# Optimization experiments

Measured on AMD Instinct MI355X. Metric: run time of the kernel, lower is better.

Reference implementation:

```python
import jax, jax.numpy as jnp
import numpy as np
from jax import lax

CUT = 20            # voxel grid per side, hard-coded in the torch module
N, P, OP = 32, 8192, 2048


def _w(key, shape, fan_in):
    return jax.random.normal(key, shape, dtype=jnp.float32) * np.float32(1.0 / np.sqrt(fan_in))


def setup_inputs() -> dict:
    key = jax.random.key(0)
    ks = jax.random.split(key, 20)
    inp = {}
    inp["sc"] = jax.random.uniform(ks[0], (N, P, 2), dtype=jnp.float32, minval=-0.5, maxval=0.5)
    inp["oc"] = jax.random.uniform(ks[1], (N, OP, 2), dtype=jnp.float32, minval=-0.5, maxval=0.5)
    inp["pos"] = jax.random.uniform(ks[2], (N, 2), dtype=jnp.float32, minval=-0.5, maxval=0.5)
    # voxel PointNet MLP (1x1 Conv1d == per-point linear)
    inp["mlp_w1"] = _w(ks[3], (128, 2), 2);        inp["mlp_b1"] = jnp.zeros((128,), jnp.float32)
    inp["mlp_w2"] = _w(ks[4], (256, 128), 128);    inp["mlp_b2"] = jnp.zeros((256,), jnp.float32)
    # dense conv pyramid
    inp["conv1_w"] = _w(ks[5], (512, 256, 3, 3), 256 * 9);   inp["conv1_b"] = jnp.zeros((512,), jnp.float32)
    inp["conv2_w"] = _w(ks[6], (1024, 512, 3, 3), 512 * 9);  inp["conv2_b"] = jnp.zeros((1024,), jnp.float32)
    inp["convt_w"] = _w(ks[7], (512, 1024, 2, 2), 1024 * 4); inp["convt_b"] = jnp.zeros((512,), jnp.float32)
    # object set-abstraction (stack of 1x1 Conv1d)
    inp["sa_w1"] = _w(ks[8], (64, 2), 2);          inp["sa_b1"] = jnp.zeros((64,), jnp.float32)
    inp["sa_w2"] = _w(ks[9], (128, 64), 64);       inp["sa_b2"] = jnp.zeros((128,), jnp.float32)
    inp["sa_w3"] = _w(ks[10], (256, 128), 128);    inp["sa_b3"] = jnp.zeros((256,), jnp.float32)
    inp["sa_w4"] = _w(ks[11], (512, 256), 256);    inp["sa_b4"] = jnp.zeros((512,), jnp.float32)
    # per-cell classifier
    inp["cls_w1"] = _w(ks[12], (1024, 1538), 1538); inp["cls_b1"] = jnp.zeros((1024,), jnp.float32)
    inp["cls_w2"] = _w(ks[13], (256, 1024), 1024);  inp["cls_b2"] = jnp.zeros((256,), jnp.float32)
    inp["cls_w3"] = _w(ks[14], (1, 256), 256);      inp["cls_b3"] = jnp.zeros((1,), jnp.float32)
    return inp


def _conv2d(x, w, b):
    y = lax.conv_general_dilated(x, w, (1, 1), ((1, 1), (1, 1)),
                                 dimension_numbers=("NCHW", "OIHW", "NCHW"))
    return y + b[None, :, None, None]


def _maxpool2(x):
    return lax.reduce_window(x, -jnp.inf, lax.max, (1, 1, 2, 2), (1, 1, 2, 2), "VALID")


def reference(sc, oc, pos,
              mlp_w1, mlp_b1, mlp_w2, mlp_b2,
              conv1_w, conv1_b, conv2_w, conv2_b, convt_w, convt_b,
              sa_w1, sa_b1, sa_w2, sa_b2, sa_w3, sa_b3, sa_w4, sa_b4,
              cls_w1, cls_b1, cls_w2, cls_b2, cls_w3, cls_b3):
    n = sc.shape[0]
    # ---- fused voxelization + PointNet + scatter-max (replaces triple loop) ----
    x, y = sc[..., 0], sc[..., 1]
    # torch condition: cut[i] < x <= cut[i+1] on linspace(-0.5, 0.5, 21)
    bi = jnp.clip(jnp.ceil((x + 0.5) * CUT) - 1, 0, CUT - 1).astype(jnp.int32)
    bj = jnp.clip(jnp.ceil((y + 0.5) * CUT) - 1, 0, CUT - 1).astype(jnp.int32)
    valid = (x > -0.5) & (x <= 0.5) & (y > -0.5) & (y <= 0.5)
    ci = -0.5 + (bi.astype(sc.dtype) + 0.5) / CUT   # voxel center x
    cj = -0.5 + (bj.astype(sc.dtype) + 0.5) / CUT   # voxel center y
    pc = jnp.stack([x - ci, y - cj], axis=-1).reshape(-1, 2)        # [n*P, 2]
    h = jax.nn.relu(pc @ mlp_w1.T + mlp_b1)
    feat = jax.nn.relu(h @ mlp_w2.T + mlp_b2)                       # [n*P, 256]
    seg = jnp.where(valid,
                    jnp.arange(n, dtype=jnp.int32)[:, None] * (CUT * CUT) + bi * CUT + bj,
                    n * CUT * CUT).reshape(-1)                      # invalid -> dummy bin
    nseg = n * CUT * CUT + 1
    mx = jax.ops.segment_max(feat, seg, num_segments=nseg)
    cnt = jax.ops.segment_sum(jnp.ones((n * P,), jnp.float32), seg, num_segments=nseg)
    vox = jnp.where(cnt[:, None] > 0, mx, 0.0)[: n * CUT * CUT]     # empty voxels stay 0
    vox = vox.reshape(n, CUT, CUT, 256).transpose(0, 3, 1, 2)       # [n,256,20,20]
    # ---- dense conv pyramid ----
    f1 = _maxpool2(jax.nn.relu(_conv2d(vox, conv1_w, conv1_b)))     # [n,512,10,10]
    f2 = _maxpool2(jax.nn.relu(_conv2d(f1, conv2_w, conv2_b)))      # [n,1024,5,5]
    f3 = lax.conv_transpose(f2, convt_w, (2, 2), "VALID",
                            dimension_numbers=("NCHW", "OIHW", "NCHW"))
    f3 = f3 + convt_b[None, :, None, None]                          # [n,512,10,10]
    scene = jnp.concatenate([f1, f3], axis=1)                       # [n,1024,10,10]
    S = scene.shape[2]
    scene_flat = scene.reshape(n, 1024, S * S)
    # ---- object PointNet (1x1 convs == per-point linears) + global max ----
    obj_c = oc - jnp.mean(oc, axis=1, keepdims=True)                # [n,OP,2]
    g = jax.nn.relu(obj_c @ sa_w1.T + sa_b1)
    g = jax.nn.relu(g @ sa_w2.T + sa_b2)
    g = jax.nn.relu(g @ sa_w3.T + sa_b3)
    g = jax.nn.relu(g @ sa_w4.T + sa_b4)                            # [n,OP,512]
    obj = jnp.max(g, axis=1)                                        # [n,512]
    obj_tiled = jnp.broadcast_to(obj[:, :, None], (n, 512, S * S))
    # ---- relative position grid ----
    c = -0.5 + (jnp.arange(S, dtype=sc.dtype) + 0.5) / S
    rel_x = jnp.broadcast_to(pos[:, 0][:, None, None] - c[None, :, None], (n, S, S))
    rel_y = jnp.broadcast_to(pos[:, 1][:, None, None] - c[None, None, :], (n, S, S))
    rel = jnp.stack([rel_x, rel_y], axis=1).reshape(n, 2, S * S)
    # ---- per-cell classifier ----
    cin = jnp.concatenate([scene_flat, obj_tiled, rel], axis=1).transpose(0, 2, 1)  # [n,100,1538]
    h = jax.nn.relu(cin @ cls_w1.T + cls_b1)
    h = jax.nn.relu(h @ cls_w2.T + cls_b2)
    return h @ cls_w3.T + cls_b3                                    # [n,100,1]
```

## Files before the change

### kernel.cpp

```cpp
#include <hip/hip_runtime.h>

#define NB 32
#define PP 8192
#define OPP 2048

typedef _Float16 f16;
typedef f16 half8 __attribute__((ext_vector_type(8)));
typedef f16 half4 __attribute__((ext_vector_type(4)));
typedef f16 half2v __attribute__((ext_vector_type(2)));
typedef float f32x4 __attribute__((ext_vector_type(4)));

#define MFMA16(a, b, c) __builtin_amdgcn_mfma_f32_16x16x32_f16(a, b, c, 0, 0, 0)

template <int CO, int CI>
__global__ __launch_bounds__(256) void wfragprep_k(const float* __restrict__ wsrc,
                                                   f16* __restrict__ wf) {
  __shared__ float tile[CI * 9];
  int co = blockIdx.x, t = threadIdx.x;
  const float* src = wsrc + (size_t)co * CI * 9;
  for (int i = t; i < CI * 9; i += 256) tile[i] = src[i];
  __syncthreads();
  constexpr int NBB = CO / 16;
  int nb = co >> 4, l16 = co & 15;
  for (int e = t; e < (CI / 32) * 9 * 4; e += 256) {
    int quad = e & 3;
    int kk = (e >> 2) % 9;
    int cic = e / 36;
    half8 v;
#pragma unroll
    for (int j = 0; j < 8; ++j) {
      int ci = cic * 32 + quad * 8 + j;
      v[j] = (f16)tile[ci * 9 + kk];
    }
    *(half8*)(wf + ((((size_t)cic * 9 + kk) * NBB + nb) * 64 + quad * 16 + l16) * 8) = v;
  }
}

__global__ void cvt16_k(const float* __restrict__ in, f16* __restrict__ out, int n4) {
  int idx = blockIdx.x * 256 + threadIdx.x;
  if (idx >= n4) return;
  float4 v = ((const float4*)in)[idx];
  half4 h; h.x = (f16)v.x; h.y = (f16)v.y; h.z = (f16)v.z; h.w = (f16)v.w;
  ((half4*)out)[idx] = h;
}

__global__ void cw1prep_k(const float* __restrict__ w, f16* __restrict__ out) {
  int idx = blockIdx.x * 256 + threadIdx.x;
  if (idx >= 1024 * 1024) return;
  int co = idx >> 10, k = idx & 1023;
  out[idx] = (f16)w[(size_t)co * 1538 + k];
}

__global__ void ctprep_k(const float* __restrict__ w, f16* __restrict__ out) {
  int idx = blockIdx.x * 256 + threadIdx.x;
  if (idx >= 2048 * 1024) return;
  int j = idx & 7, l = (idx >> 3) & 63, kb = (idx >> 9) & 31, nb = idx >> 14;
  int n16 = l & 15, quad = l >> 4;
  int np = nb * 16 + n16;
  int k = kb * 32 + quad * 8 + j;
  int p = np >> 9, o = np & 511;
  out[idx] = (f16)w[((size_t)o * 1024 + k) * 4 + (3 - p)];
}

__global__ void ocmean_k(const float* __restrict__ oc, float* __restrict__ ocm) {
  int n = blockIdx.x, t = threadIdx.x;
  __shared__ float sx[256], sy[256];
  float ax = 0.f, ay = 0.f;
  for (int p = t; p < OPP; p += 256) {
    ax += oc[((size_t)n * OPP + p) * 2 + 0];
    ay += oc[((size_t)n * OPP + p) * 2 + 1];
  }
  sx[t] = ax; sy[t] = ay;
  __syncthreads();
  for (int s = 128; s > 0; s >>= 1) {
    if (t < s) { sx[t] += sx[t + s]; sy[t] += sy[t + s]; }
    __syncthreads();
  }
  if (t == 0) {
    ocm[n * 2 + 0] = sx[0] / (float)OPP;
    ocm[n * 2 + 1] = sy[0] / (float)OPP;
  }
}

__global__ __launch_bounds__(256) void pointnet_lds_k(
    const float* __restrict__ sc, const float* __restrict__ w1, const float* __restrict__ b1,
    const f16* __restrict__ w2h, const float* __restrict__ b2, float* __restrict__ voxg) {
  __shared__ float voxl[400 * 33];
  int t = threadIdx.x, lane = t & 63, w = t >> 6;
  int quad = lane >> 4, l16 = lane & 15;
  int b = blockIdx.x;
  int ps = b & 3, cg = (b >> 2) & 7, n = b >> 5;
  half2v w1x2[16], w1y2[16], b12[16];
#pragma unroll
  for (int i = 0; i < 16; ++i) {
    int k0 = (i >> 2) * 32 + quad * 8 + (i & 3) * 2;
    w1x2[i] = (half2v){(f16)w1[k0 * 2], (f16)w1[(k0 + 1) * 2]};
    w1y2[i] = (half2v){(f16)w1[k0 * 2 + 1], (f16)w1[(k0 + 1) * 2 + 1]};
    b12[i]  = (half2v){(f16)b1[k0], (f16)b1[k0 + 1]};
  }
  half8 bf[2][4];
  float bias[2];
#pragma unroll
  for (int nt = 0; nt < 2; ++nt) {
    int ch = cg * 32 + nt * 16 + l16;
    bias[nt] = b2[ch];
#pragma unroll
    for (int ks = 0; ks < 4; ++ks)
      bf[nt][ks] = *(const half8*)(w2h + (size_t)ch * 128 + ks * 32 + quad * 8);
  }
  for (int i = t; i < 400 * 33; i += 256) voxl[i] = 0.0f;
  __syncthreads();
  const half2v z2 = {};
  const float* scp = sc + ((size_t)n * PP + (size_t)ps * 2048) * 2;
  int p0 = w * 16 + l16;
  float2 xy = *(const float2*)(scp + p0 * 2);
  for (int it = 0; it < 32; ++it) {
    float x = xy.x, y = xy.y;
    if (it < 31) xy = *(const float2*)(scp + ((it + 1) * 64 + p0) * 2);
    float bif = fminf(fmaxf(ceilf((x + 0.5f) * 20.0f) - 1.0f, 0.0f), 19.0f);
    float bjf = fminf(fmaxf(ceilf((y + 0.5f) * 20.0f) - 1.0f, 0.0f), 19.0f);
    bool valid = (x > -0.5f) && (x <= 0.5f) && (y > -0.5f) && (y <= 0.5f);
    float px = x - (-0.5f + (bif + 0.5f) * 0.05f);
    float py = y - (-0.5f + (bjf + 0.5f) * 0.05f);
    int bn = valid ? ((int)bif * 20 + (int)bjf) : -1;
    f16 pxh = (f16)px, pyh = (f16)py;
    half2v px2 = (half2v){pxh, pxh}, py2 = (half2v){pyh, pyh};
    f32x4 acc0 = {}, acc1 = {};
#pragma unroll
    for (int ks = 0; ks < 4; ++ks) {
      half8 af;
#pragma unroll
      for (int j2 = 0; j2 < 4; ++j2) {
        half2v tmp = w1x2[ks * 4 + j2] * px2 + (w1y2[ks * 4 + j2] * py2 + b12[ks * 4 + j2]);
        tmp = __builtin_elementwise_max(tmp, z2);
        reinterpret_cast<half2v*>(&af)[j2] = tmp;
      }
      acc0 = MFMA16(af, bf[0][ks], acc0);
      acc1 = MFMA16(af, bf[1][ks], acc1);
    }
#pragma unroll
    for (int r = 0; r < 4; ++r) {
      int bn2 = __shfl(bn, quad * 4 + r);
      if (bn2 >= 0) {
        float v0 = fmaxf(acc0[r] + bias[0], 0.0f);
        float v1 = fmaxf(acc1[r] + bias[1], 0.0f);
        atomicMax((int*)voxl + bn2 * 33 + l16, __float_as_int(v0));
        atomicMax((int*)voxl + bn2 * 33 + 16 + l16, __float_as_int(v1));
      }
    }
  }
  __syncthreads();
  float* vg = voxg + ((size_t)n * 400) * 256 + cg * 32;
  for (int i = t; i < 400 * 32; i += 256) {
    int bin = i >> 5, c = i & 31;
    float v = voxl[bin * 33 + c];
    if (v > 0.0f)
      atomicMax((int*)(vg + (size_t)bin * 256) + c, __float_as_int(v));
  }
}

template <int H, int W, int CI, int CO, int MSPLIT>
__global__ __launch_bounds__(256, 2) void convmfma_k(
    const f16* __restrict__ inh, const f16* __restrict__ wf,
    const float* __restrict__ bias, f16* __restrict__ outh) {
  constexpr int HS = H / MSPLIT;
  constexpr int Mpix = HS * W;
  constexpr int MT = (Mpix + 15) / 16;
  constexpr int PR = HS + 2, PC = W + 2;
  constexpr int NCIC = CI / 32;
  constexpr int COG = CO / 128;
  constexpr int NBB = CO / 16;
  extern __shared__ char smem[];
  f16* Ap = (f16*)smem;
  int b = blockIdx.x;
  int cog = b % COG;
  int ms = (b / COG) % MSPLIT;
  int n = b / (COG * MSPLIT);
  int co0 = cog * 128;
  int r0 = ms * HS;
  int t = threadIdx.x, lane = t & 63, w = t >> 6;
  int quad = lane >> 4, l16 = lane & 15;
  int nb0 = cog * 8 + w * 2;

  int abase[MT];
#pragma unroll
  for (int mi = 0; mi < MT; ++mi) {
    int pl = mi * 16 + l16; if (pl > Mpix - 1) pl = Mpix - 1;
    int y = pl / W, x = pl - y * W;
    abase[mi] = (y * PC + x) * 40 + quad * 8;
  }
  f32x4 acc[MT][2] = {};

  const f16* inbase = inh + (size_t)n * H * W * CI;

  for (int cic = 0; cic < NCIC; ++cic) {
    __syncthreads();
    for (int cell = t; cell < PR * PC; cell += 256) {
      int pr = cell / PC, pc = cell - pr * PC;
      int yin = r0 - 1 + pr, xin = pc - 1;
      uint4 d0 = {0,0,0,0}, d1 = {0,0,0,0}, d2 = {0,0,0,0}, d3 = {0,0,0,0};
      if (yin >= 0 && yin < H && xin >= 0 && xin < W) {
        const uint4* src = (const uint4*)(inbase + ((size_t)yin * W + xin) * CI + cic * 32);
        d0 = src[0]; d1 = src[1]; d2 = src[2]; d3 = src[3];
      }
      uint4* dst = (uint4*)(Ap + cell * 40);
      dst[0] = d0; dst[1] = d1; dst[2] = d2; dst[3] = d3;
    }
    __syncthreads();
    const f16* wfc = wf + (size_t)(cic * 9) * NBB * 512;
#pragma unroll
    for (int ky = 0; ky < 3; ++ky)
#pragma unroll
      for (int kx = 0; kx < 3; ++kx) {
        int kk = ky * 3 + kx;
        half8 bf0 = *(const half8*)(wfc + ((size_t)(kk * NBB + nb0) * 64 + lane) * 8);
        half8 bf1 = *(const half8*)(wfc + ((size_t)(kk * NBB + nb0 + 1) * 64 + lane) * 8);
        int shift = (ky * PC + kx) * 40;
#pragma unroll
        for (int mi = 0; mi < MT; ++mi) {
          half8 af = *(const half8*)(Ap + abase[mi] + shift);
          acc[mi][0] = MFMA16(af, bf0, acc[mi][0]);
          acc[mi][1] = MFMA16(af, bf1, acc[mi][1]);
        }
      }
  }
  int co_w = co0 + w * 32;
  float bv0 = bias[co_w + l16];
  float bv1 = bias[co_w + 16 + l16];
  f16* ob = outh + ((size_t)n * H * W + (size_t)ms * Mpix) * CO;
#pragma unroll
  for (int mi = 0; mi < MT; ++mi) {
#pragma unroll
    for (int r = 0; r < 4; ++r) {
      int p = mi * 16 + quad * 4 + r;
      if (p < Mpix) {
        float v0 = acc[mi][0][r] + bv0; v0 = v0 > 0.f ? v0 : 0.f;
        float v1 = acc[mi][1][r] + bv1; v1 = v1 > 0.f ? v1 : 0.f;
        ob[(size_t)p * CO + co_w + l16] = (f16)v0;
        ob[(size_t)p * CO + co_w + 16 + l16] = (f16)v1;
      }
    }
  }
}

__global__ void pool1_k(const f16* __restrict__ g1, f16* __restrict__ f1h,
                        f16* __restrict__ scnh) {
  int idx = blockIdx.x * 256 + threadIdx.x;
  if (idx >= 32 * 100 * 256) return;
  int c2 = idx & 255, rem = idx >> 8;
  int op = rem % 100, n = rem / 100;
  int py = op / 10, px = op - py * 10;
  const f16* base = g1 + (((size_t)n * 400 + (size_t)(2 * py) * 20 + 2 * px) * 512) + c2 * 2;
  float a0 = (float)base[0],   a1 = (float)base[1];
  float b0 = (float)base[512], b1 = (float)base[513];
  const f16* base2 = base + 20 * 512;
  float c0 = (float)base2[0],   c1 = (float)base2[1];
  float d0 = (float)base2[512], d1 = (float)base2[513];
  union { f16 h[2]; unsigned u; } pk;
  pk.h[0] = (f16)fmaxf(fmaxf(a0, b0), fmaxf(c0, d0));
  pk.h[1] = (f16)fmaxf(fmaxf(a1, b1), fmaxf(c1, d1));
  *(unsigned*)(f1h + ((size_t)n * 100 + op) * 512 + c2 * 2) = pk.u;
  *(unsigned*)(scnh + ((size_t)n * 100 + op) * 1024 + c2 * 2) = pk.u;
}

__global__ void pool2_k(const f16* __restrict__ g2, f16* __restrict__ f2h) {
  int idx = blockIdx.x * 256 + threadIdx.x;
  if (idx >= 32 * 25 * 512) return;
  int c2 = idx & 511, rem = idx >> 9;
  int op = rem % 25, n = rem / 25;
  int py = op / 5, px = op - py * 5;
  const f16* base = g2 + (((size_t)n * 100 + (size_t)(2 * py) * 10 + 2 * px) * 1024) + c2 * 2;
  float a0 = (float)base[0],    a1 = (float)base[1];
  float b0 = (float)base[1024], b1 = (float)base[1025];
  const f16* base2 = base + 10 * 1024;
  float c0 = (float)base2[0],    c1 = (float)base2[1];
  float d0 = (float)base2[1024], d1 = (float)base2[1025];
  f16* o = f2h + ((size_t)n * 25 + op) * 1024 + c2 * 2;
  o[0] = (f16)fmaxf(fmaxf(a0, b0), fmaxf(c0, d0));
  o[1] = (f16)fmaxf(fmaxf(a1, b1), fmaxf(c1, d1));
}

__global__ __launch_bounds__(256, 2) void convt_mfma_k(
    const f16* __restrict__ f2h, const f16* __restrict__ ctwf,
    const float* __restrict__ ctb, f16* __restrict__ scnh) {
  __shared__ f16 act[25 * 1048];
  int b = blockIdx.x;
  int ng = b & 15, n = b >> 4;
  int t = threadIdx.x, lane = t & 63, w = t >> 6;
  int quad = lane >> 4, l16 = lane & 15;
  for (int i = t; i < 25 * 128; i += 256) {
    int row = i >> 7, c8 = i & 127;
    *(half8*)(act + row * 1048 + c8 * 8) =
        *(const half8*)(f2h + ((size_t)n * 25 + row) * 1024 + c8 * 8);
  }
  __syncthreads();
  int r1 = 16 + (l16 > 8 ? 8 : l16);
  f32x4 acc[2][2] = {};
  const f16* wp0 = ctwf + ((size_t)((ng * 8 + w * 2 + 0) * 32) * 64 + lane) * 8;
  const f16* wp1 = ctwf + ((size_t)((ng * 8 + w * 2 + 1) * 32) * 64 + lane) * 8;
#pragma unroll 4
  for (int ks = 0; ks < 32; ++ks) {
    half8 a0 = *(const half8*)(act + l16 * 1048 + ks * 32 + quad * 8);
    half8 a1 = *(const half8*)(act + r1 * 1048 + ks * 32 + quad * 8);
    half8 b0 = *(const half8*)(wp0 + (size_t)ks * 512);
    half8 b1 = *(const half8*)(wp1 + (size_t)ks * 512);
    acc[0][0] = MFMA16(a0, b0, acc[0][0]);
    acc[1][0] = MFMA16(a1, b0, acc[1][0]);
    acc[0][1] = MFMA16(a0, b1, acc[0][1]);
    acc[1][1] = MFMA16(a1, b1, acc[1][1]);
  }
#pragma unroll
  for (int nt = 0; nt < 2; ++nt) {
    int np = ng * 128 + w * 32 + nt * 16 + l16;
    int p = np >> 9, co = np & 511;
    int a = p >> 1, bc = p & 1;
    float bb = ctb[co];
#pragma unroll
    for (int mt = 0; mt < 2; ++mt)
#pragma unroll
      for (int r = 0; r < 4; ++r) {
        int px = mt * 16 + quad * 4 + r;
        if (px < 25) {
          int ph = px / 5, pw = px - ph * 5;
          int opx = (2 * ph + a) * 10 + 2 * pw + bc;
          scnh[((size_t)n * 100 + opx) * 1024 + 512 + co] = (f16)(acc[mt][nt][r] + bb);
        }
      }
  }
}

__global__ __launch_bounds__(256, 2) void sa_mfma_k(
    const float* __restrict__ oc, const float* __restrict__ ocm,
    const float* __restrict__ w1, const float* __restrict__ b1,
    const f16* __restrict__ w2h, const float* __restrict__ b2,
    const f16* __restrict__ w3h, const float* __restrict__ b3,
    const f16* __restrict__ w4h, const float* __restrict__ b4,
    float* __restrict__ obj) {
  __shared__ f16 act1[64 * 72];
  __shared__ f16 act2[64 * 136];
  __shared__ f16 act3[64 * 264];
  __shared__ float pcx[64], pcy[64];
  int b = blockIdx.x;
  int n = b >> 5, pb = (b & 31) * 64;
  int t = threadIdx.x, lane = t & 63, w = t >> 6;
  int quad = lane >> 4, l16 = lane & 15;
  if (t < 64) {
    pcx[t] = oc[((size_t)n * OPP + pb + t) * 2 + 0] - ocm[n * 2 + 0];
    pcy[t] = oc[((size_t)n * OPP + pb + t) * 2 + 1] - ocm[n * 2 + 1];
  }
  __syncthreads();
  {
    int c = t & 63, pg = t >> 6;
    float wx = w1[c * 2], wy = w1[c * 2 + 1], bb = b1[c];
#pragma unroll
    for (int j = 0; j < 16; ++j) {
      int p = pg * 16 + j;
      act1[p * 72 + c] = (f16)fmaxf(fmaf(wx, pcx[p], fmaf(wy, pcy[p], bb)), 0.0f);
    }
  }
  __syncthreads();
  {
    int n0 = w * 32;
    f32x4 acc[4][2] = {};
#pragma unroll
    for (int ks = 0; ks < 2; ++ks) {
      half8 a[4];
#pragma unroll
      for (int mt = 0; mt < 4; ++mt)
        a[mt] = *(const half8*)(act1 + (mt * 16 + l16) * 72 + ks * 32 + quad * 8);
#pragma unroll
      for (int nt = 0; nt < 2; ++nt) {
        half8 bf = *(const half8*)(w2h + (size_t)(n0 + nt * 16 + l16) * 64 + ks * 32 + quad * 8);
#pragma unroll
        for (int mt = 0; mt < 4; ++mt)
          acc[mt][nt] = MFMA16(a[mt], bf, acc[mt][nt]);
      }
    }
#pragma unroll
    for (int nt = 0; nt < 2; ++nt) {
      int col = n0 + nt * 16 + l16;
      float bb = b2[col];
#pragma unroll
      for (int mt = 0; mt < 4; ++mt)
#pragma unroll
        for (int r = 0; r < 4; ++r)
          act2[(mt * 16 + quad * 4 + r) * 136 + col] = (f16)fmaxf(acc[mt][nt][r] + bb, 0.0f);
    }
  }
  __syncthreads();
  {
    int n0 = w * 64;
    f32x4 acc[4][4] = {};
#pragma unroll
    for (int ks = 0; ks < 4; ++ks) {
      half8 a[4];
#pragma unroll
      for (int mt = 0; mt < 4; ++mt)
        a[mt] = *(const half8*)(act2 + (mt * 16 + l16) * 136 + ks * 32 + quad * 8);
#pragma unroll
      for (int nt = 0; nt < 4; ++nt) {
        half8 bf = *(const half8*)(w3h + (size_t)(n0 + nt * 16 + l16) * 128 + ks * 32 + quad * 8);
#pragma unroll
        for (int mt = 0; mt < 4; ++mt)
          acc[mt][nt] = MFMA16(a[mt], bf, acc[mt][nt]);
      }
    }
#pragma unroll
    for (int nt = 0; nt < 4; ++nt) {
      int col = n0 + nt * 16 + l16;
      float bb = b3[col];
#pragma unroll
      for (int mt = 0; mt < 4; ++mt)
#pragma unroll
        for (int r = 0; r < 4; ++r)
          act3[(mt * 16 + quad * 4 + r) * 264 + col] = (f16)fmaxf(acc[mt][nt][r] + bb, 0.0f);
    }
  }
  __syncthreads();
  {
    int n0 = w * 128;
    f32x4 acc[4][8] = {};
#pragma unroll
    for (int ks = 0; ks < 8; ++ks) {
      half8 a[4];
#pragma unroll
      for (int mt = 0; mt < 4; ++mt)
        a[mt] = *(const half8*)(act3 + (mt * 16 + l16) * 264 + ks * 32 + quad * 8);
#pragma unroll
      for (int nt = 0; nt < 8; ++nt) {
        half8 bf = *(const half8*)(w4h + (size_t)(n0 + nt * 16 + l16) * 256 + ks * 32 + quad * 8);
#pragma unroll
        for (int mt = 0; mt < 4; ++mt)
          acc[mt][nt] = MFMA16(a[mt], bf, acc[mt][nt]);
      }
    }
#pragma unroll
    for (int nt = 0; nt < 8; ++nt) {
      int col = n0 + nt * 16 + l16;
      float bb = b4[col];
      float v = 0.0f;
#pragma unroll
      for (int mt = 0; mt < 4; ++mt)
#pragma unroll
        for (int r = 0; r < 4; ++r)
          v = fmaxf(v, acc[mt][nt][r] + bb);
      v = fmaxf(v, 0.0f);
      v = fmaxf(v, __shfl_xor(v, 16));
      v = fmaxf(v, __shfl_xor(v, 32));
      if (quad == 0)
        atomicMax((int*)obj + (size_t)n * 512 + col, __float_as_int(v));
    }
  }
}

__global__ __launch_bounds__(256) void cls1_mfma_k(
    const f16* __restrict__ scnh, const float* __restrict__ obj,
    const float* __restrict__ pos, const float* __restrict__ w1raw,
    const f16* __restrict__ w1h, const float* __restrict__ b1,
    f16* __restrict__ h1h) {
  __shared__ f16 act[32 * 72];
  __shared__ float objl[512];
  __shared__ float odl[128], wAl[128], wBl[128];
  int b = blockIdx.x;
  int mq = b & 3, o8 = (b >> 2) & 7, n = b >> 5;
  int co0 = o8 * 128, p0 = mq * 25;
  int t = threadIdx.x, lane = t & 63, w = t >> 6;
  int quad = lane >> 4, l16 = lane & 15;
  objl[t] = obj[(size_t)n * 512 + t];
  objl[t + 256] = obj[(size_t)n * 512 + t + 256];
  __syncthreads();
  {
    int co = co0 + (t >> 1);
    int kh = (t & 1) * 256;
    const float* wr = w1raw + (size_t)co * 1538 + 1024 + kh;
    float od = 0.0f;
    for (int k = 0; k < 256; ++k) od = fmaf(objl[kh + k], wr[k], od);
    od += __shfl_xor(od, 1);
    if ((t & 1) == 0) {
      odl[t >> 1] = od + b1[co];
      wAl[t >> 1] = w1raw[(size_t)co * 1538 + 1536];
      wBl[t >> 1] = w1raw[(size_t)co * 1538 + 1537];
    }
  }
  __syncthreads();
  float posx = pos[n * 2 + 0], posy = pos[n * 2 + 1];
  f32x4 acc[2][2];
#pragma unroll
  for (int mt = 0; mt < 2; ++mt)
#pragma unroll
    for (int nt = 0; nt < 2; ++nt) {
      int cl = w * 32 + nt * 16 + l16;
      float od = odl[cl], wA = wAl[cl], wB = wBl[cl];
#pragma unroll
      for (int r = 0; r < 4; ++r) {
        int pl = mt * 16 + quad * 4 + r;
        int px = p0 + (pl < 25 ? pl : 24);
        float relx = posx - (-0.5f + ((px / 10) + 0.5f) * 0.1f);
        float rely = posy - (-0.5f + ((px % 10) + 0.5f) * 0.1f);
        acc[mt][nt][r] = od + relx * wA + rely * wB;
      }
    }
  for (int kc = 0; kc < 16; ++kc) {
    int k0 = kc * 64;
    __syncthreads();
    {
      int row = t >> 3, c8 = t & 7;
      int gr = p0 + (row < 25 ? row : 24);
      *(half8*)(act + row * 72 + c8 * 8) =
          *(const half8*)(scnh + ((size_t)n * 100 + gr) * 1024 + k0 + c8 * 8);
    }
    __syncthreads();
#pragma unroll
    for (int ks = 0; ks < 2; ++ks) {
      half8 bf0 = *(const half8*)(w1h + (size_t)(co0 + w * 32 + l16) * 1024 + k0 + ks * 32 + quad * 8);
      half8 bf1 = *(const half8*)(w1h + (size_t)(co0 + w * 32 + 16 + l16) * 1024 + k0 + ks * 32 + quad * 8);
#pragma unroll
      for (int mt = 0; mt < 2; ++mt) {
        half8 a = *(const half8*)(act + (mt * 16 + l16) * 72 + ks * 32 + quad * 8);
        acc[mt][0] = MFMA16(a, bf0, acc[mt][0]);
        acc[mt][1] = MFMA16(a, bf1, acc[mt][1]);
      }
    }
  }
#pragma unroll
  for (int mt = 0; mt < 2; ++mt)
#pragma unroll
    for (int nt = 0; nt < 2; ++nt) {
      int co = co0 + w * 32 + nt * 16 + l16;
#pragma unroll
      for (int r = 0; r < 4; ++r) {
        int pl = mt * 16 + quad * 4 + r;
        if (pl < 25)
          h1h[((size_t)n * 100 + p0 + pl) * 1024 + co] = (f16)fmaxf(acc[mt][nt][r], 0.0f);
      }
    }
}

__global__ __launch_bounds__(256) void cls2_mfma_k(
    const f16* __restrict__ h1h, const f16* __restrict__ w2h16,
    const float* __restrict__ b2, f16* __restrict__ h2h) {
  __shared__ f16 act[64 * 72];
  int b = blockIdx.x;
  int ng = b & 1, mh = (b >> 1) & 1, n = b >> 2;
  int co0 = ng * 128, p0 = mh * 50;
  int t = threadIdx.x, lane = t & 63, w = t >> 6;
  int quad = lane >> 4, l16 = lane & 15;
  f32x4 acc[4][2] = {};
  for (int kc = 0; kc < 16; ++kc) {
    int k0 = kc * 64;
    __syncthreads();
    for (int i = t; i < 512; i += 256) {
      int row = i >> 3, c8 = i & 7;
      int gr = p0 + (row < 50 ? row : 49);
      *(half8*)(act + row * 72 + c8 * 8) =
          *(const half8*)(h1h + ((size_t)n * 100 + gr) * 1024 + k0 + c8 * 8);
    }
    __syncthreads();
#pragma unroll
    for (int ks = 0; ks < 2; ++ks) {
      half8 bf0 = *(const half8*)(w2h16 + (size_t)(co0 + w * 32 + l16) * 1024 + k0 + ks * 32 + quad * 8);
      half8 bf1 = *(const half8*)(w2h16 + (size_t)(co0 + w * 32 + 16 + l16) * 1024 + k0 + ks * 32 + quad * 8);
#pragma unroll
      for (int mt = 0; mt < 4; ++mt) {
        half8 a = *(const half8*)(act + (mt * 16 + l16) * 72 + ks * 32 + quad * 8);
        acc[mt][0] = MFMA16(a, bf0, acc[mt][0]);
        acc[mt][1] = MFMA16(a, bf1, acc[mt][1]);
      }
    }
  }
#pragma unroll
  for (int mt = 0; mt < 4; ++mt)
#pragma unroll
    for (int nt = 0; nt < 2; ++nt) {
      int co = co0 + w * 32 + nt * 16 + l16;
      float bb = b2[co];
#pragma unroll
      for (int r = 0; r < 4; ++r) {
        int pl = mt * 16 + quad * 4 + r;
        if (pl < 50)
          h2h[((size_t)n * 100 + p0 + pl) * 256 + co] = (f16)fmaxf(acc[mt][nt][r] + bb, 0.0f);
      }
    }
}

__global__ void cls3_k(const f16* __restrict__ h2h, const float* __restrict__ w3,
                       const float* __restrict__ b3, float* __restrict__ out) {
  int n = blockIdx.x, t = threadIdx.x;
  if (t < 100) {
    float acc = b3[0];
    const f16* hp = &h2h[((size_t)n * 100 + t) * 256];
    for (int k = 0; k < 256; ++k) acc = fmaf((float)hp[k], w3[k], acc);
    out[n * 100 + t] = acc;
  }
}

extern "C" void kernel_launch(void* const* d_in, const int* in_sizes, int n_in,
                              void* d_out, int out_size, void* d_ws, size_t ws_size,
                              hipStream_t stream) {
  const float* sc      = (const float*)d_in[0];
  const float* oc      = (const float*)d_in[1];
  const float* pos     = (const float*)d_in[2];
  const float* mlp_w1  = (const float*)d_in[3];
  const float* mlp_b1  = (const float*)d_in[4];
  const float* mlp_w2  = (const float*)d_in[5];
  const float* mlp_b2  = (const float*)d_in[6];
  const float* conv1_w = (const float*)d_in[7];
  const float* conv1_b = (const float*)d_in[8];
  const float* conv2_w = (const float*)d_in[9];
  const float* conv2_b = (const float*)d_in[10];
  const float* convt_w = (const float*)d_in[11];
  const float* convt_b = (const float*)d_in[12];
  const float* sa_w1   = (const float*)d_in[13];
  const float* sa_b1   = (const float*)d_in[14];
  const float* sa_w2   = (const float*)d_in[15];
  const float* sa_b2   = (const float*)d_in[16];
  const float* sa_w3   = (const float*)d_in[17];
  const float* sa_b3   = (const float*)d_in[18];
  const float* sa_w4   = (const float*)d_in[19];
  const float* sa_b4   = (const float*)d_in[20];
  const float* cls_w1  = (const float*)d_in[21];
  const float* cls_b1  = (const float*)d_in[22];
  const float* cls_w2  = (const float*)d_in[23];
  const float* cls_b2  = (const float*)d_in[24];
  const float* cls_w3  = (const float*)d_in[25];
  const float* cls_b3  = (const float*)d_in[26];

  float* ws = (float*)d_ws;
  f16*   w1h   = (f16*)ws;
  f16*   w2h   = (f16*)(ws + 589824);
  f16*   mw2h  = (f16*)(ws + 2949120);
  f16*   saw2h = (f16*)(ws + 2965504);
  f16*   saw3h = (f16*)(ws + 2969600);
  f16*   saw4h = (f16*)(ws + 2985984);
  f16*   cw1h  = (f16*)(ws + 3051520);
  f16*   ctwh  = (f16*)(ws + 3575808);
  f16*   cw2h  = (f16*)(ws + 4624384);
  float* big   = ws + 4886528;
  f16*   voxh  = (f16*)(ws + 8163328);
  f16*   f1h   = (f16*)(ws + 8982528);
  f16*   scnh  = (f16*)(ws + 9801728);
  float* obj   = ws + 11440128;
  float* ocm   = ws + 11456512;

  float* voxg  = big;
  f16*   g1buf = (f16*)big;
  f16*   g2buf = (f16*)big;
  f16*   f2h   = voxh;
  f16*   h1h   = w2h;
  f16*   h2h   = scnh;
  float* outp  = (float*)d_out;

  wfragprep_k<512, 256><<<512, 256, 0, stream>>>(conv1_w, w1h);
  wfragprep_k<1024, 512><<<1024, 256, 0, stream>>>(conv2_w, w2h);
  cvt16_k<<<32, 256, 0, stream>>>(mlp_w2, mw2h, 8192);
  cvt16_k<<<8, 256, 0, stream>>>(sa_w2, saw2h, 2048);
  cvt16_k<<<32, 256, 0, stream>>>(sa_w3, saw3h, 8192);
  cvt16_k<<<128, 256, 0, stream>>>(sa_w4, saw4h, 32768);
  cw1prep_k<<<4096, 256, 0, stream>>>(cls_w1, cw1h);
  ctprep_k<<<8192, 256, 0, stream>>>(convt_w, ctwh);
  cvt16_k<<<256, 256, 0, stream>>>(cls_w2, cw2h, 65536);

  hipMemsetAsync(obj, 0, (size_t)16384 * 4, stream);
  hipMemsetAsync(voxg, 0, (size_t)3276800 * 4, stream);
  ocmean_k<<<32, 256, 0, stream>>>(oc, ocm);

  pointnet_lds_k<<<1024, 256, 0, stream>>>(sc, mlp_w1, mlp_b1, mw2h, mlp_b2, voxg);
  cvt16_k<<<3200, 256, 0, stream>>>(voxg, voxh, 819200);

  convmfma_k<20, 20, 256, 512, 4><<<512, 256, 7 * 22 * 80, stream>>>(
      voxh, w1h, conv1_b, g1buf);
  pool1_k<<<3200, 256, 0, stream>>>(g1buf, f1h, scnh);
  convmfma_k<10, 10, 512, 1024, 2><<<512, 256, 7 * 12 * 80, stream>>>(
      f1h, w2h, conv2_b, g2buf);
  pool2_k<<<1600, 256, 0, stream>>>(g2buf, f2h);
  convt_mfma_k<<<512, 256, 0, stream>>>(f2h, ctwh, convt_b, scnh);

  sa_mfma_k<<<1024, 256, 0, stream>>>(oc, ocm, sa_w1, sa_b1, saw2h, sa_b2,
                                      saw3h, sa_b3, saw4h, sa_b4, obj);

  cls1_mfma_k<<<1024, 256, 0, stream>>>(scnh, obj, pos, cls_w1, cw1h, cls_b1, h1h);
  cls2_mfma_k<<<128, 256, 0, stream>>>(h1h, cw2h, cls_b2, h2h);
  cls3_k<<<32, 128, 0, stream>>>(h2h, cls_w3, cls_b3, outp);
}
```

Measured before the change: 514.7 us.

## Stage full activation tile once in cls1 and use wave-parallel obj dot

The cls1 kernel now loads the whole 25x1024 activation slice into LDS once, instead of 16 chunked loads each bracketed by two barriers. The K loop then runs MFMAs directly from that buffer with no synchronization. The object-feature dot product is rewritten so each wave reduces one output channel at a time, using coalesced float2 loads and shuffle reductions, and the LDS staging of obj is dropped. The cost is about 51KB of LDS per block, which may reduce occupancy.

```diff
diff --git a/kernel.cpp b/kernel.cpp
--- a/kernel.cpp
+++ b/kernel.cpp
@@ -458,28 +458,39 @@
     const float* __restrict__ pos, const float* __restrict__ w1raw,
     const f16* __restrict__ w1h, const float* __restrict__ b1,
     f16* __restrict__ h1h) {
-  __shared__ f16 act[32 * 72];
-  __shared__ float objl[512];
+  __shared__ f16 act[25 * 1032];
   __shared__ float odl[128], wAl[128], wBl[128];
   int b = blockIdx.x;
   int mq = b & 3, o8 = (b >> 2) & 7, n = b >> 5;
   int co0 = o8 * 128, p0 = mq * 25;
   int t = threadIdx.x, lane = t & 63, w = t >> 6;
   int quad = lane >> 4, l16 = lane & 15;
-  objl[t] = obj[(size_t)n * 512 + t];
-  objl[t + 256] = obj[(size_t)n * 512 + t + 256];
-  __syncthreads();
+  for (int i = t; i < 25 * 128; i += 256) {
+    int row = i >> 7, c8 = i & 127;
+    *(half8*)(act + row * 1032 + c8 * 8) =
+        *(const half8*)(scnh + ((size_t)n * 100 + p0 + row) * 1024 + c8 * 8);
+  }
   {
-    int co = co0 + (t >> 1);
-    int kh = (t & 1) * 256;
-    const float* wr = w1raw + (size_t)co * 1538 + 1024 + kh;
-    float od = 0.0f;
-    for (int k = 0; k < 256; ++k) od = fmaf(objl[kh + k], wr[k], od);
-    od += __shfl_xor(od, 1);
-    if ((t & 1) == 0) {
-      odl[t >> 1] = od + b1[co];
-      wAl[t >> 1] = w1raw[(size_t)co * 1538 + 1536];
-      wBl[t >> 1] = w1raw[(size_t)co * 1538 + 1537];
+    const float* ob = obj + (size_t)n * 512;
+    for (int i = 0; i < 32; ++i) {
+      int co = co0 + w * 32 + i;
+      const float* wr = w1raw + (size_t)co * 1538 + 1024;
+      float od = 0.0f;
+#pragma unroll
+      for (int j = 0; j < 4; ++j) {
+        float2 wv = *(const float2*)(wr + lane * 8 + j * 2);
+        float2 ov = *(const float2*)(ob + lane * 8 + j * 2);
+        od = fmaf(wv.x, ov.x, od);
+        od = fmaf(wv.y, ov.y, od);
+      }
+      od += __shfl_xor(od, 1);  od += __shfl_xor(od, 2);
+      od += __shfl_xor(od, 4);  od += __shfl_xor(od, 8);
+      od += __shfl_xor(od, 16); od += __shfl_xor(od, 32);
+      if (lane == 0) {
+        odl[w * 32 + i] = od + b1[co];
+        wAl[w * 32 + i] = wr[512];
+        wBl[w * 32 + i] = wr[513];
+      }
     }
   }
   __syncthreads();
@@ -500,27 +511,21 @@
         acc[mt][nt][r] = od + relx * wA + rely * wB;
       }
     }
-  for (int kc = 0; kc < 16; ++kc) {
-    int k0 = kc * 64;
-    __syncthreads();
-    {
-      int row = t >> 3, c8 = t & 7;
-      int gr = p0 + (row < 25 ? row : 24);
-      *(half8*)(act + row * 72 + c8 * 8) =
-          *(const half8*)(scnh + ((size_t)n * 100 + gr) * 1024 + k0 + c8 * 8);
-    }
-    __syncthreads();
-#pragma unroll
-    for (int ks = 0; ks < 2; ++ks) {
-      half8 bf0 = *(const half8*)(w1h + (size_t)(co0 + w * 32 + l16) * 1024 + k0 + ks * 32 + quad * 8);
-      half8 bf1 = *(const half8*)(w1h + (size_t)(co0 + w * 32 + 16 + l16) * 1024 + k0 + ks * 32 + quad * 8);
-#pragma unroll
-      for (int mt = 0; mt < 2; ++mt) {
-        half8 a = *(const half8*)(act + (mt * 16 + l16) * 72 + ks * 32 + quad * 8);
-        acc[mt][0] = MFMA16(a, bf0, acc[mt][0]);
-        acc[mt][1] = MFMA16(a, bf1, acc[mt][1]);
-      }
-    }
+  int gr0 = l16;
+  int gr1 = (16 + l16 > 24) ? 24 : 16 + l16;
+  const f16* wb0 = w1h + (size_t)(co0 + w * 32 + l16) * 1024 + quad * 8;
+  const f16* wb1 = wb0 + (size_t)16 * 1024;
+#pragma unroll 4
+  for (int kq = 0; kq < 32; ++kq) {
+    int k0 = kq * 32;
+    half8 bf0 = *(const half8*)(wb0 + k0);
+    half8 bf1 = *(const half8*)(wb1 + k0);
+    half8 a0 = *(const half8*)(act + gr0 * 1032 + k0 + quad * 8);
+    half8 a1 = *(const half8*)(act + gr1 * 1032 + k0 + quad * 8);
+    acc[0][0] = MFMA16(a0, bf0, acc[0][0]);
+    acc[1][0] = MFMA16(a1, bf0, acc[1][0]);
+    acc[0][1] = MFMA16(a0, bf1, acc[0][1]);
+    acc[1][1] = MFMA16(a1, bf1, acc[1][1]);
   }
 #pragma unroll
   for (int mt = 0; mt < 2; ++mt)
```

Measured after the change: 525.3 us. 2.1% more time.
